# Kernel optimization log

Hardware: AMD Instinct MI355X
Metric: run time of the kernel (lower is better)

Reference implementation:

```python
import jax, jax.numpy as jnp
import numpy as np

N, CH, H, W = 4, 512, 64, 64
FEAT, NUM_K, POOL_PER = 256, 64, 128
POOL = NUM_K * POOL_PER  # 8192 total concept slots


def setup_inputs() -> dict:
    key = jax.random.key(0)
    k_x, k_t, k_o, k_p = jax.random.split(key, 4)
    x = jax.random.normal(k_x, (N, CH, H, W), dtype=jnp.float32)
    # 1x1 conv weights stored as [out, in] matrices (kernel_size=1, bias=False)
    w_theta = jax.random.normal(k_t, (FEAT, CH), dtype=jnp.float32) * 0.02
    w_o = jax.random.normal(k_o, (CH, FEAT), dtype=jnp.float32) * 0.02
    # concept pool buffer initialized with torch.rand -> uniform [0, 1)
    concept_pool = jax.random.uniform(k_p, (FEAT, POOL), dtype=jnp.float32)
    gamma = jnp.float32(0.5)  # learned scalar gate (init 0.0 in module; 0.5 to exercise the path)
    return {"x": x, "w_theta": w_theta, "w_o": w_o, "concept_pool": concept_pool, "gamma": gamma}


def reference(x, w_theta, w_o, concept_pool, gamma):
    # Concept attention: queries from theta 1x1 conv, keys/values are the
    # external concept pool memory [feature_dim, total_pool_size].
    n, c, h, w = x.shape
    hw = h * w
    # theta 1x1 conv: [n, ch, h, w] -> [n, feat, hw]
    theta = jnp.einsum('nchw,fc->nfhw', x, w_theta).reshape(n, FEAT, hw)
    # attention logits over pool slots: [n, hw, pool]
    logits = jnp.einsum('nfl,fp->nlp', theta, concept_pool)
    attn = jax.nn.softmax(logits, axis=-1)
    # aggregate pool values: [n, feat, hw]
    agg = jnp.einsum('nlp,fp->nfl', attn, concept_pool).reshape(n, FEAT, h, w)
    # output 1x1 conv back to ch, gated residual
    o = jnp.einsum('nfhw,cf->nchw', agg, w_o)
    return x + gamma * o
```

## Files before the change

kernel.cpp:

```cpp
#include <hip/hip_runtime.h>

#define NB 4
#define CHN 512
#define HWD 4096
#define LTOT (NB*HWD)
#define FEAT_ 256
#define POOL_ 8192

typedef __attribute__((ext_vector_type(8))) __bf16 bf16x8;
typedef __attribute__((ext_vector_type(8))) unsigned short u16x8;
typedef __attribute__((ext_vector_type(8))) _Float16 f16x8;
typedef __attribute__((ext_vector_type(4))) float f32x4;
typedef __attribute__((ext_vector_type(16))) float f32x16;

static __device__ __forceinline__ unsigned short f2bf(float f){
  union { float f; unsigned u; } c; c.f = f;
  unsigned u = c.u;
  u += 0x7fffu + ((u >> 16) & 1u);
  return (unsigned short)(u >> 16);
}

static __device__ __forceinline__ unsigned pk_f16(float lo, float hi){
  auto r = __builtin_amdgcn_cvt_pkrtz(lo, hi);
  return __builtin_bit_cast(unsigned, r);
}

static __device__ __forceinline__ f32x4 mfma16(bf16x8 a, bf16x8 b, f32x4 c){
  return __builtin_amdgcn_mfma_f32_16x16x32_bf16(a, b, c, 0, 0, 0);
}
static __device__ __forceinline__ f32x4 mfma16h(f16x8 a, f16x8 b, f32x4 c){
  return __builtin_amdgcn_mfma_f32_16x16x32_f16(a, b, c, 0, 0, 0);
}
static __device__ __forceinline__ f32x16 mfma32h(f16x8 a, f16x8 b, f32x16 c){
  return __builtin_amdgcn_mfma_f32_32x32x16_f16(a, b, c, 0, 0, 0);
}

static __device__ __forceinline__ bf16x8 ld_bf8(const void* p){
  u16x8 v = *(const u16x8*)p;
  return __builtin_bit_cast(bf16x8, v);
}
static __device__ __forceinline__ f16x8 ld_f8(const void* p){
  u16x8 v = *(const u16x8*)p;
  return __builtin_bit_cast(f16x8, v);
}

static __device__ __forceinline__ void gload16(const void* g, void* l){
  __builtin_amdgcn_global_load_lds((const __attribute__((address_space(1))) void*)g,
                                   (__attribute__((address_space(3))) void*)l, 16, 0, 0);
}

__global__ void k_cvt(const float* __restrict__ src, unsigned short* __restrict__ dst, int n4){
  int i = blockIdx.x * 256 + threadIdx.x;
  if (i < n4) {
    const float4 v = *(const float4*)(src + (size_t)i * 4);
    ushort4 o; o.x = f2bf(v.x); o.y = f2bf(v.y); o.z = f2bf(v.z); o.w = f2bf(v.w);
    *(ushort4*)(dst + (size_t)i * 4) = o;
  }
}

__global__ __launch_bounds__(256) void k_poolKF(const float* __restrict__ pool,
                                                unsigned short* __restrict__ poolKF){
  int t = blockIdx.x >> 2;
  int tid = threadIdx.x;
  int kk = ((blockIdx.x & 3) << 1) | (tid >> 7);
  int half = (tid >> 6) & 1;
  int lane = tid & 63;
  int p = t*32 + half*16 + (lane & 15);
  int f0 = kk*32 + ((lane >> 4) & 3)*8;
  u16x8 o;
  #pragma unroll
  for (int j = 0; j < 8; ++j) o[j] = f2bf(pool[(size_t)(f0+j)*POOL_ + p]);
  *(u16x8*)((char*)poolKF + (size_t)t*16384 + (kk*2+half)*1024 + lane*16) = o;
}

__global__ __launch_bounds__(256) void k_poolVF(const float* __restrict__ pool,
                                                _Float16* __restrict__ poolVF){
  int t = blockIdx.x >> 2;
  int tid = threadIdx.x;
  int g = ((blockIdx.x & 3) << 2) | (tid >> 6);
  int lane = tid & 63;
  int f = (g & 7)*32 + (lane & 31);
  int sb = ((g >> 3) << 4) + ((lane >> 5) << 3);
  f16x8 o;
  #pragma unroll
  for (int j = 0; j < 8; ++j) {
    int s = sb + j;
    int po = (s >> 1) + ((s & 1) << 4);
    o[j] = (_Float16)pool[(size_t)f*POOL_ + t*32 + po];
  }
  *(f16x8*)((char*)poolVF + (size_t)t*16384 + g*1024 + lane*16) = o;
}

__global__ __launch_bounds__(256) void k_xT(const float* __restrict__ x,
                                            unsigned short* __restrict__ xT){
  __shared__ float tile[32][33];
  int b = blockIdx.x;
  int lt = b & 127; int ct = (b >> 7) & 15; int n = b >> 11;
  int t = threadIdx.x;
  int fi = t >> 3, j = (t & 7) * 4;
  const float4 v = *(const float4*)(x + ((size_t)(n*CHN + ct*32 + fi)) * HWD + lt*32 + j);
  tile[fi][j+0] = v.x; tile[fi][j+1] = v.y; tile[fi][j+2] = v.z; tile[fi][j+3] = v.w;
  __syncthreads();
  int pi = t >> 3, fj = (t & 7) * 4;
  ushort4 o;
  o.x = f2bf(tile[fj+0][pi]); o.y = f2bf(tile[fj+1][pi]);
  o.z = f2bf(tile[fj+2][pi]); o.w = f2bf(tile[fj+3][pi]);
  *(ushort4*)((char*)xT + ((size_t)(n*HWD + lt*32 + pi)) * 1024 + (ct*32 + fj) * 2) = o;
}

__global__ __launch_bounds__(256) void k_theta(const unsigned short* __restrict__ xT,
                                               const unsigned short* __restrict__ wt,
                                               unsigned short* __restrict__ Q){
  int w = threadIdx.x >> 6, lane = threadIdx.x & 63;
  int lq = lane & 15, hq = lane >> 4;
  int lbase = blockIdx.x * 64 + w * 16;
  const char* xb = (const char*)xT;
  const char* wb = (const char*)wt;
  f32x4 acc[16];
  #pragma unroll
  for (int i = 0; i < 16; ++i) acc[i] = {};
  #pragma unroll 2
  for (int kk = 0; kk < 16; ++kk) {
    bf16x8 a = ld_bf8(xb + (size_t)(lbase + lq) * 1024 + kk*64 + hq*16);
    #pragma unroll
    for (int fi = 0; fi < 16; ++fi) {
      bf16x8 bfr = ld_bf8(wb + (size_t)(fi*16 + lq) * 1024 + kk*64 + hq*16);
      acc[fi] = mfma16(a, bfr, acc[fi]);
    }
  }
  #pragma unroll
  for (int fi = 0; fi < 16; ++fi) {
    #pragma unroll
    for (int r = 0; r < 4; ++r) {
      int l = lbase + hq*4 + r;
      Q[(size_t)l * 256 + fi*16 + lq] = f2bf(acc[fi][r]);
    }
  }
}

__global__ __launch_bounds__(256, 2) void k_attn(const unsigned short* __restrict__ Qg,
                                                 const unsigned short* __restrict__ poolKF,
                                                 const _Float16* __restrict__ poolVF,
                                                 _Float16* __restrict__ accP,
                                                 float* __restrict__ pm,
                                                 float* __restrict__ ps){
  __shared__ __attribute__((aligned(16))) unsigned short K_lds[2][32*256];
  __shared__ __attribute__((aligned(16))) _Float16 V_lds[2][8192];
  __shared__ __attribute__((aligned(16))) _Float16 P_lds[4][32][40];
  __shared__ float Sc[4][32];
  __shared__ float As[4][32];

  int w = threadIdx.x >> 6, lane = threadIdx.x & 63;
  int lq = lane & 15, hq = lane >> 4;
  int ln = lane & 31, h2 = lane >> 5;
  int qblock = blockIdx.x & 127, slice = blockIdx.x >> 7;
  int qa0 = qblock * 128 + w * 32;

  const char* qp = (const char*)Qg;
  bf16x8 qfa[8], qfb[8];
  #pragma unroll
  for (int kk = 0; kk < 8; ++kk) {
    qfa[kk] = ld_bf8(qp + (size_t)(qa0 + lq) * 512 + kk*64 + hq*16);
    qfb[kk] = ld_bf8(qp + (size_t)(qa0 + 16 + lq) * 512 + kk*64 + hq*16);
  }

  f32x16 acc32[8];
  #pragma unroll
  for (int i = 0; i < 8; ++i) acc32[i] = {};
  f32x4 accsA = {}, accsB = {};
  float ma0 = -__builtin_inff(), ma1 = -__builtin_inff(),
        ma2 = -__builtin_inff(), ma3 = -__builtin_inff();
  float mb0 = -__builtin_inff(), mb1 = -__builtin_inff(),
        mb2 = -__builtin_inff(), mb3 = -__builtin_inff();
  u16x8 ov;
  #pragma unroll
  for (int i = 0; i < 8; ++i) ov[i] = 0x3C00;
  const f16x8 ONESH = __builtin_bit_cast(f16x8, ov);

  const char* ktb = (const char*)poolKF;
  const char* vnb = (const char*)poolVF;
  int kds[4];
  #pragma unroll
  for (int i = 0; i < 4; ++i) kds[i] = (w*4 + i) * 1024;
  int lsrc = lane * 16;
  _Float16 (*Pw)[40] = P_lds[w];

  {
    size_t tb = (size_t)(slice * 64) * 16384;
    #pragma unroll
    for (int i = 0; i < 4; ++i) {
      gload16(ktb + tb + kds[i] + lsrc, (char*)K_lds[0] + kds[i]);
      gload16(vnb + tb + kds[i] + lsrc, (char*)V_lds[0] + kds[i]);
    }
  }
  __syncthreads();

  int cur = 0;
  for (int t = 0; t < 64; ++t) {
    if (t < 63) {
      size_t tb = (size_t)(slice*64 + t + 1) * 16384;
      #pragma unroll
      for (int i = 0; i < 4; ++i) {
        gload16(ktb + tb + kds[i] + lsrc, (char*)K_lds[cur^1] + kds[i]);
        gload16(vnb + tb + kds[i] + lsrc, (char*)V_lds[cur^1] + kds[i]);
      }
    }

    const char* Kb = (const char*)K_lds[cur] + lsrc;
    const char* Vb = (const char*)V_lds[cur] + lsrc;

    f32x4 s0a = {}, s1a = {}, s0b = {}, s1b = {};
    #pragma unroll
    for (int kk = 0; kk < 8; ++kk) {
      bf16x8 k0 = ld_bf8(Kb + kk*2048);
      bf16x8 k1 = ld_bf8(Kb + kk*2048 + 1024);
      s0a = mfma16(qfa[kk], k0, s0a);
      s1a = mfma16(qfa[kk], k1, s1a);
      s0b = mfma16(qfb[kk], k0, s0b);
      s1b = mfma16(qfb[kk], k1, s1b);
    }

    float pa0 = fmaxf(s0a[0], s1a[0]), pa1 = fmaxf(s0a[1], s1a[1]),
          pa2 = fmaxf(s0a[2], s1a[2]), pa3 = fmaxf(s0a[3], s1a[3]);
    float pb0 = fmaxf(s0b[0], s1b[0]), pb1 = fmaxf(s0b[1], s1b[1]),
          pb2 = fmaxf(s0b[2], s1b[2]), pb3 = fmaxf(s0b[3], s1b[3]);
    bool ex = (pa0 > ma0+4.f) | (pa1 > ma1+4.f) | (pa2 > ma2+4.f) | (pa3 > ma3+4.f) |
              (pb0 > mb0+4.f) | (pb1 > mb1+4.f) | (pb2 > mb2+4.f) | (pb3 > mb3+4.f);
    if (__any((int)ex)) {
      #pragma unroll
      for (int msk = 1; msk < 16; msk <<= 1) {
        pa0 = fmaxf(pa0, __shfl_xor(pa0, msk));
        pa1 = fmaxf(pa1, __shfl_xor(pa1, msk));
        pa2 = fmaxf(pa2, __shfl_xor(pa2, msk));
        pa3 = fmaxf(pa3, __shfl_xor(pa3, msk));
        pb0 = fmaxf(pb0, __shfl_xor(pb0, msk));
        pb1 = fmaxf(pb1, __shfl_xor(pb1, msk));
        pb2 = fmaxf(pb2, __shfl_xor(pb2, msk));
        pb3 = fmaxf(pb3, __shfl_xor(pb3, msk));
      }
      float na0 = fmaxf(ma0, pa0), na1 = fmaxf(ma1, pa1),
            na2 = fmaxf(ma2, pa2), na3 = fmaxf(ma3, pa3);
      float nb0 = fmaxf(mb0, pb0), nb1 = fmaxf(mb1, pb1),
            nb2 = fmaxf(mb2, pb2), nb3 = fmaxf(mb3, pb3);
      float sa0 = __expf(ma0 - na0), sa1 = __expf(ma1 - na1),
            sa2 = __expf(ma2 - na2), sa3 = __expf(ma3 - na3);
      float sb0 = __expf(mb0 - nb0), sb1 = __expf(mb1 - nb1),
            sb2 = __expf(mb2 - nb2), sb3 = __expf(mb3 - nb3);
      ma0 = na0; ma1 = na1; ma2 = na2; ma3 = na3;
      mb0 = nb0; mb1 = nb1; mb2 = nb2; mb3 = nb3;
      accsA[0] *= sa0; accsA[1] *= sa1; accsA[2] *= sa2; accsA[3] *= sa3;
      accsB[0] *= sb0; accsB[1] *= sb1; accsB[2] *= sb2; accsB[3] *= sb3;
      if (lq == 0) {
        Sc[w][4*hq+0] = sa0; Sc[w][4*hq+1] = sa1;
        Sc[w][4*hq+2] = sa2; Sc[w][4*hq+3] = sa3;
        Sc[w][16+4*hq+0] = sb0; Sc[w][16+4*hq+1] = sb1;
        Sc[w][16+4*hq+2] = sb2; Sc[w][16+4*hq+3] = sb3;
      }
      f32x4 s4[4];
      #pragma unroll
      for (int blk = 0; blk < 4; ++blk)
        s4[blk] = *(const f32x4*)&Sc[w][8*blk + 4*h2];
      #pragma unroll
      for (int fb = 0; fb < 8; ++fb)
        #pragma unroll
        for (int r = 0; r < 16; ++r)
          acc32[fb][r] *= s4[r>>2][r&3];
    }

    {
      int q0 = hq * 4;
      *(unsigned*)&Pw[q0+0][lq*2] = pk_f16(__expf(s0a[0]-ma0), __expf(s1a[0]-ma0));
      *(unsigned*)&Pw[q0+1][lq*2] = pk_f16(__expf(s0a[1]-ma1), __expf(s1a[1]-ma1));
      *(unsigned*)&Pw[q0+2][lq*2] = pk_f16(__expf(s0a[2]-ma2), __expf(s1a[2]-ma2));
      *(unsigned*)&Pw[q0+3][lq*2] = pk_f16(__expf(s0a[3]-ma3), __expf(s1a[3]-ma3));
      *(unsigned*)&Pw[16+q0+0][lq*2] = pk_f16(__expf(s0b[0]-mb0), __expf(s1b[0]-mb0));
      *(unsigned*)&Pw[16+q0+1][lq*2] = pk_f16(__expf(s0b[1]-mb1), __expf(s1b[1]-mb1));
      *(unsigned*)&Pw[16+q0+2][lq*2] = pk_f16(__expf(s0b[2]-mb2), __expf(s1b[2]-mb2));
      *(unsigned*)&Pw[16+q0+3][lq*2] = pk_f16(__expf(s0b[3]-mb3), __expf(s1b[3]-mb3));
    }

    f16x8 paA = ld_f8(&Pw[lq][hq*8]);
    f16x8 paB = ld_f8(&Pw[16+lq][hq*8]);
    accsA = mfma16h(paA, ONESH, accsA);
    accsB = mfma16h(paB, ONESH, accsB);

    #pragma unroll
    for (int ph = 0; ph < 2; ++ph) {
      f16x8 pfrag = ld_f8(&Pw[ln][ph*16 + h2*8]);
      #pragma unroll
      for (int fb = 0; fb < 8; ++fb) {
        f16x8 vfrag = ld_f8(Vb + (ph*8 + fb)*1024);
        acc32[fb] = mfma32h(pfrag, vfrag, acc32[fb]);
      }
    }

    __syncthreads();
    cur ^= 1;
  }

  if (lq == 0) {
    As[w][4*hq+0] = accsA[0]; As[w][4*hq+1] = accsA[1];
    As[w][4*hq+2] = accsA[2]; As[w][4*hq+3] = accsA[3];
    As[w][16+4*hq+0] = accsB[0]; As[w][16+4*hq+1] = accsB[1];
    As[w][16+4*hq+2] = accsB[2]; As[w][16+4*hq+3] = accsB[3];
  }
  float inv[16];
  #pragma unroll
  for (int blk = 0; blk < 4; ++blk) {
    f32x4 a4 = *(const f32x4*)&As[w][8*blk + 4*h2];
    inv[blk*4+0] = 1.0f / a4[0]; inv[blk*4+1] = 1.0f / a4[1];
    inv[blk*4+2] = 1.0f / a4[2]; inv[blk*4+3] = 1.0f / a4[3];
  }
  size_t sbase = (size_t)slice * 16384 + qa0;
  #pragma unroll
  for (int fb = 0; fb < 8; ++fb) {
    #pragma unroll
    for (int r = 0; r < 16; ++r) {
      int q = (r & 3) + 8*(r >> 2) + 4*h2;
      accP[(sbase + q) * 256 + fb*32 + ln] = (_Float16)(acc32[fb][r] * inv[r]);
    }
  }
  if (lq == 0) {
    pm[sbase + 4*hq + 0] = ma0; ps[sbase + 4*hq + 0] = accsA[0];
    pm[sbase + 4*hq + 1] = ma1; ps[sbase + 4*hq + 1] = accsA[1];
    pm[sbase + 4*hq + 2] = ma2; ps[sbase + 4*hq + 2] = accsA[2];
    pm[sbase + 4*hq + 3] = ma3; ps[sbase + 4*hq + 3] = accsA[3];
    pm[sbase + 16 + 4*hq + 0] = mb0; ps[sbase + 16 + 4*hq + 0] = accsB[0];
    pm[sbase + 16 + 4*hq + 1] = mb1; ps[sbase + 16 + 4*hq + 1] = accsB[1];
    pm[sbase + 16 + 4*hq + 2] = mb2; ps[sbase + 16 + 4*hq + 2] = accsB[2];
    pm[sbase + 16 + 4*hq + 3] = mb3; ps[sbase + 16 + 4*hq + 3] = accsB[3];
  }
}

__global__ __launch_bounds__(256) void k_comb(const _Float16* __restrict__ accP,
                                              const float* __restrict__ pm,
                                              const float* __restrict__ ps,
                                              unsigned short* __restrict__ agg){
  int q = blockIdx.x * 16 + (threadIdx.x >> 4);
  int f0 = (threadIdx.x & 15) * 16;
  float m0 = pm[q], m1 = pm[16384 + q], m2 = pm[2*16384 + q], m3 = pm[3*16384 + q];
  float M = fmaxf(fmaxf(m0, m1), fmaxf(m2, m3));
  float w0 = __expf(m0 - M) * ps[q];
  float w1 = __expf(m1 - M) * ps[16384 + q];
  float w2 = __expf(m2 - M) * ps[2*16384 + q];
  float w3 = __expf(m3 - M) * ps[3*16384 + q];
  float inv = 1.0f / (w0 + w1 + w2 + w3);
  w0 *= inv; w1 *= inv; w2 *= inv; w3 *= inv;
  const _Float16* a0 = accP + (size_t)q * 256 + f0;
  #pragma unroll
  for (int j = 0; j < 16; j += 8) {
    f16x8 v0 = *(const f16x8*)(a0 + j);
    f16x8 v1 = *(const f16x8*)(a0 + j + (size_t)16384*256);
    f16x8 v2 = *(const f16x8*)(a0 + j + (size_t)2*16384*256);
    f16x8 v3 = *(const f16x8*)(a0 + j + (size_t)3*16384*256);
    u16x8 o;
    #pragma unroll
    for (int k = 0; k < 8; ++k) {
      float s = w0*(float)v0[k] + w1*(float)v1[k] + w2*(float)v2[k] + w3*(float)v3[k];
      o[k] = f2bf(s);
    }
    *(u16x8*)(agg + (size_t)q * 256 + f0 + j) = o;
  }
}

__global__ __launch_bounds__(256) void k_out(const float* __restrict__ x,
                                             const unsigned short* __restrict__ wo,
                                             const unsigned short* __restrict__ agg,
                                             const float* __restrict__ gammap,
                                             float* __restrict__ out){
  int w = threadIdx.x >> 6, lane = threadIdx.x & 63;
  int lq = lane & 15, hq = lane >> 4;
  int b = blockIdx.x;
  int lg = b & 63, cg = (b >> 6) & 7, n = b >> 9;
  const char* wb = (const char*)wo;
  const char* ab = (const char*)agg;
  f32x4 acc[4];
  #pragma unroll
  for (int i = 0; i < 4; ++i) acc[i] = {};
  int crow = cg*64 + w*16 + lq;
  #pragma unroll
  for (int kk = 0; kk < 8; ++kk) {
    bf16x8 a = ld_bf8(wb + (size_t)crow * 512 + kk*64 + hq*16);
    #pragma unroll
    for (int li = 0; li < 4; ++li) {
      bf16x8 bb = ld_bf8(ab + (size_t)(n*HWD + lg*64 + li*16 + lq) * 512 + kk*64 + hq*16);
      acc[li] = mfma16(a, bb, acc[li]);
    }
  }
  float g = gammap[0];
  #pragma unroll
  for (int li = 0; li < 4; ++li) {
    #pragma unroll
    for (int r = 0; r < 4; ++r) {
      int c = cg*64 + w*16 + hq*4 + r;
      int l = lg*64 + li*16 + lq;
      size_t idx = ((size_t)(n*CHN + c)) * HWD + l;
      out[idx] = x[idx] + g * acc[li][r];
    }
  }
}

extern "C" void kernel_launch(void* const* d_in, const int* in_sizes, int n_in,
                              void* d_out, int out_size, void* d_ws, size_t ws_size,
                              hipStream_t stream) {
  const float* x     = (const float*)d_in[0];
  const float* wt    = (const float*)d_in[1];
  const float* wo    = (const float*)d_in[2];
  const float* pool  = (const float*)d_in[3];
  const float* gamma = (const float*)d_in[4];
  char* ws = (char*)d_ws;
  unsigned short* wt_b  = (unsigned short*)(ws + 0);
  unsigned short* wo_b  = (unsigned short*)(ws + 262144);
  _Float16*       poolVF= (_Float16*)(ws + 524288);
  unsigned short* poolKF= (unsigned short*)(ws + 4718592);
  unsigned short* Qb    = (unsigned short*)(ws + 8912896);
  unsigned short* aggb  = (unsigned short*)(ws + 17301504);
  unsigned short* xT    = (unsigned short*)(ws + 25690112);
  _Float16*       accP  = (_Float16*)(ws + 25690112);
  float*          pm    = (float*)(ws + 59244544);
  float*          ps    = (float*)(ws + 59506688);
  float* out = (float*)d_out;

  k_cvt<<<dim3(128), dim3(256), 0, stream>>>(wt, wt_b, 32768);
  k_cvt<<<dim3(128), dim3(256), 0, stream>>>(wo, wo_b, 32768);
  k_poolVF<<<dim3(1024), dim3(256), 0, stream>>>(pool, poolVF);
  k_poolKF<<<dim3(1024), dim3(256), 0, stream>>>(pool, poolKF);
  k_xT<<<dim3(8192), dim3(256), 0, stream>>>(x, xT);
  k_theta<<<dim3(256), dim3(256), 0, stream>>>(xT, wt_b, Qb);
  k_attn<<<dim3(512), dim3(256), 0, stream>>>(Qb, poolKF, poolVF, accP, pm, ps);
  k_comb<<<dim3(1024), dim3(256), 0, stream>>>(accP, pm, ps, aggb);
  k_out<<<dim3(2048), dim3(256), 0, stream>>>(x, wo_b, aggb, gamma, out);
}
```

Before: 258.7 us.

## Compute S^T with 32x32 MFMA so P stays in registers, use exp2

Restructures the attention inner loop to compute transposed scores with 32x32x16 bf16 MFMA, K as the A operand and Q as B. Each lane then holds one query's scores, so softmax row max and sum need only one cross-half shuffle. Probabilities are packed straight into f16 registers as the A operand for the PV MFMA, which removes the P round trip through LDS and the ones-vector MFMA row-sum. Pool K/V pre-layouts are changed to match, and log2(e) is folded into Q so exp2 replaces expf. This cuts LDS traffic and shuffles, at the cost of a different rescale threshold and extra VALU summation.

```diff
diff --git a/kernel.cpp b/kernel.cpp
--- a/kernel.cpp
+++ b/kernel.cpp
@@ -10,8 +10,13 @@
 typedef __attribute__((ext_vector_type(8))) __bf16 bf16x8;
 typedef __attribute__((ext_vector_type(8))) unsigned short u16x8;
 typedef __attribute__((ext_vector_type(8))) _Float16 f16x8;
+typedef __attribute__((ext_vector_type(4))) unsigned u32x4;
 typedef __attribute__((ext_vector_type(4))) float f32x4;
 typedef __attribute__((ext_vector_type(16))) float f32x16;
+
+static __device__ __forceinline__ float fexp2(float x){
+  return __builtin_amdgcn_exp2f(x);
+}
 
 static __device__ __forceinline__ unsigned short f2bf(float f){
   union { float f; unsigned u; } c; c.f = f;
@@ -28,8 +33,8 @@
 static __device__ __forceinline__ f32x4 mfma16(bf16x8 a, bf16x8 b, f32x4 c){
   return __builtin_amdgcn_mfma_f32_16x16x32_bf16(a, b, c, 0, 0, 0);
 }
-static __device__ __forceinline__ f32x4 mfma16h(f16x8 a, f16x8 b, f32x4 c){
-  return __builtin_amdgcn_mfma_f32_16x16x32_f16(a, b, c, 0, 0, 0);
+static __device__ __forceinline__ f32x16 mfma32b(bf16x8 a, bf16x8 b, f32x16 c){
+  return __builtin_amdgcn_mfma_f32_32x32x16_bf16(a, b, c, 0, 0, 0);
 }
 static __device__ __forceinline__ f32x16 mfma32h(f16x8 a, f16x8 b, f32x16 c){
   return __builtin_amdgcn_mfma_f32_32x32x16_f16(a, b, c, 0, 0, 0);
@@ -62,15 +67,14 @@
                                                 unsigned short* __restrict__ poolKF){
   int t = blockIdx.x >> 2;
   int tid = threadIdx.x;
-  int kk = ((blockIdx.x & 3) << 1) | (tid >> 7);
-  int half = (tid >> 6) & 1;
+  int kc = ((blockIdx.x & 3) << 2) | (tid >> 6);
   int lane = tid & 63;
-  int p = t*32 + half*16 + (lane & 15);
-  int f0 = kk*32 + ((lane >> 4) & 3)*8;
+  int p = t*32 + (lane & 31);
+  int f0 = kc*16 + (lane >> 5)*8;
   u16x8 o;
   #pragma unroll
   for (int j = 0; j < 8; ++j) o[j] = f2bf(pool[(size_t)(f0+j)*POOL_ + p]);
-  *(u16x8*)((char*)poolKF + (size_t)t*16384 + (kk*2+half)*1024 + lane*16) = o;
+  *(u16x8*)((char*)poolKF + (size_t)t*16384 + kc*1024 + lane*16) = o;
 }
 
 __global__ __launch_bounds__(256) void k_poolVF(const float* __restrict__ pool,
@@ -80,12 +84,11 @@
   int g = ((blockIdx.x & 3) << 2) | (tid >> 6);
   int lane = tid & 63;
   int f = (g & 7)*32 + (lane & 31);
-  int sb = ((g >> 3) << 4) + ((lane >> 5) << 3);
+  int ph = g >> 3, h2 = lane >> 5;
   f16x8 o;
   #pragma unroll
   for (int j = 0; j < 8; ++j) {
-    int s = sb + j;
-    int po = (s >> 1) + ((s & 1) << 4);
+    int po = (j & 3) + 8*(j >> 2) + 4*h2 + 16*ph;
     o[j] = (_Float16)pool[(size_t)f*POOL_ + t*32 + po];
   }
   *(f16x8*)((char*)poolVF + (size_t)t*16384 + g*1024 + lane*16) = o;
@@ -133,7 +136,7 @@
     #pragma unroll
     for (int r = 0; r < 4; ++r) {
       int l = lbase + hq*4 + r;
-      Q[(size_t)l * 256 + fi*16 + lq] = f2bf(acc[fi][r]);
+      Q[(size_t)l * 256 + fi*16 + lq] = f2bf(acc[fi][r] * 1.44269504f);
     }
   }
 }
@@ -146,36 +149,25 @@
                                                  float* __restrict__ ps){
   __shared__ __attribute__((aligned(16))) unsigned short K_lds[2][32*256];
   __shared__ __attribute__((aligned(16))) _Float16 V_lds[2][8192];
-  __shared__ __attribute__((aligned(16))) _Float16 P_lds[4][32][40];
   __shared__ float Sc[4][32];
   __shared__ float As[4][32];
 
   int w = threadIdx.x >> 6, lane = threadIdx.x & 63;
-  int lq = lane & 15, hq = lane >> 4;
   int ln = lane & 31, h2 = lane >> 5;
   int qblock = blockIdx.x & 127, slice = blockIdx.x >> 7;
   int qa0 = qblock * 128 + w * 32;
 
   const char* qp = (const char*)Qg;
-  bf16x8 qfa[8], qfb[8];
-  #pragma unroll
-  for (int kk = 0; kk < 8; ++kk) {
-    qfa[kk] = ld_bf8(qp + (size_t)(qa0 + lq) * 512 + kk*64 + hq*16);
-    qfb[kk] = ld_bf8(qp + (size_t)(qa0 + 16 + lq) * 512 + kk*64 + hq*16);
-  }
+  bf16x8 qf[16];
+  #pragma unroll
+  for (int kc = 0; kc < 16; ++kc)
+    qf[kc] = ld_bf8(qp + (size_t)(qa0 + ln) * 512 + kc*32 + h2*16);
 
   f32x16 acc32[8];
   #pragma unroll
   for (int i = 0; i < 8; ++i) acc32[i] = {};
-  f32x4 accsA = {}, accsB = {};
-  float ma0 = -__builtin_inff(), ma1 = -__builtin_inff(),
-        ma2 = -__builtin_inff(), ma3 = -__builtin_inff();
-  float mb0 = -__builtin_inff(), mb1 = -__builtin_inff(),
-        mb2 = -__builtin_inff(), mb3 = -__builtin_inff();
-  u16x8 ov;
-  #pragma unroll
-  for (int i = 0; i < 8; ++i) ov[i] = 0x3C00;
-  const f16x8 ONESH = __builtin_bit_cast(f16x8, ov);
+  float accs = 0.0f;
+  float m = -__builtin_inff();
 
   const char* ktb = (const char*)poolKF;
   const char* vnb = (const char*)poolVF;
@@ -183,7 +175,6 @@
   #pragma unroll
   for (int i = 0; i < 4; ++i) kds[i] = (w*4 + i) * 1024;
   int lsrc = lane * 16;
-  _Float16 (*Pw)[40] = P_lds[w];
 
   {
     size_t tb = (size_t)(slice * 64) * 16384;
@@ -209,53 +200,29 @@
     const char* Kb = (const char*)K_lds[cur] + lsrc;
     const char* Vb = (const char*)V_lds[cur] + lsrc;
 
-    f32x4 s0a = {}, s1a = {}, s0b = {}, s1b = {};
-    #pragma unroll
-    for (int kk = 0; kk < 8; ++kk) {
-      bf16x8 k0 = ld_bf8(Kb + kk*2048);
-      bf16x8 k1 = ld_bf8(Kb + kk*2048 + 1024);
-      s0a = mfma16(qfa[kk], k0, s0a);
-      s1a = mfma16(qfa[kk], k1, s1a);
-      s0b = mfma16(qfb[kk], k0, s0b);
-      s1b = mfma16(qfb[kk], k1, s1b);
-    }
-
-    float pa0 = fmaxf(s0a[0], s1a[0]), pa1 = fmaxf(s0a[1], s1a[1]),
-          pa2 = fmaxf(s0a[2], s1a[2]), pa3 = fmaxf(s0a[3], s1a[3]);
-    float pb0 = fmaxf(s0b[0], s1b[0]), pb1 = fmaxf(s0b[1], s1b[1]),
-          pb2 = fmaxf(s0b[2], s1b[2]), pb3 = fmaxf(s0b[3], s1b[3]);
-    bool ex = (pa0 > ma0+4.f) | (pa1 > ma1+4.f) | (pa2 > ma2+4.f) | (pa3 > ma3+4.f) |
-              (pb0 > mb0+4.f) | (pb1 > mb1+4.f) | (pb2 > mb2+4.f) | (pb3 > mb3+4.f);
-    if (__any((int)ex)) {
-      #pragma unroll
-      for (int msk = 1; msk < 16; msk <<= 1) {
-        pa0 = fmaxf(pa0, __shfl_xor(pa0, msk));
-        pa1 = fmaxf(pa1, __shfl_xor(pa1, msk));
-        pa2 = fmaxf(pa2, __shfl_xor(pa2, msk));
-        pa3 = fmaxf(pa3, __shfl_xor(pa3, msk));
-        pb0 = fmaxf(pb0, __shfl_xor(pb0, msk));
-        pb1 = fmaxf(pb1, __shfl_xor(pb1, msk));
-        pb2 = fmaxf(pb2, __shfl_xor(pb2, msk));
-        pb3 = fmaxf(pb3, __shfl_xor(pb3, msk));
-      }
-      float na0 = fmaxf(ma0, pa0), na1 = fmaxf(ma1, pa1),
-            na2 = fmaxf(ma2, pa2), na3 = fmaxf(ma3, pa3);
-      float nb0 = fmaxf(mb0, pb0), nb1 = fmaxf(mb1, pb1),
-            nb2 = fmaxf(mb2, pb2), nb3 = fmaxf(mb3, pb3);
-      float sa0 = __expf(ma0 - na0), sa1 = __expf(ma1 - na1),
-            sa2 = __expf(ma2 - na2), sa3 = __expf(ma3 - na3);
-      float sb0 = __expf(mb0 - nb0), sb1 = __expf(mb1 - nb1),
-            sb2 = __expf(mb2 - nb2), sb3 = __expf(mb3 - nb3);
-      ma0 = na0; ma1 = na1; ma2 = na2; ma3 = na3;
-      mb0 = nb0; mb1 = nb1; mb2 = nb2; mb3 = nb3;
-      accsA[0] *= sa0; accsA[1] *= sa1; accsA[2] *= sa2; accsA[3] *= sa3;
-      accsB[0] *= sb0; accsB[1] *= sb1; accsB[2] *= sb2; accsB[3] *= sb3;
-      if (lq == 0) {
-        Sc[w][4*hq+0] = sa0; Sc[w][4*hq+1] = sa1;
-        Sc[w][4*hq+2] = sa2; Sc[w][4*hq+3] = sa3;
-        Sc[w][16+4*hq+0] = sb0; Sc[w][16+4*hq+1] = sb1;
-        Sc[w][16+4*hq+2] = sb2; Sc[w][16+4*hq+3] = sb3;
-      }
+    f32x16 Sa = {}, Sb = {};
+    #pragma unroll
+    for (int kc = 0; kc < 8; ++kc) {
+      bf16x8 k0 = ld_bf8(Kb + (2*kc)*1024);
+      bf16x8 k1 = ld_bf8(Kb + (2*kc+1)*1024);
+      Sa = mfma32b(k0, qf[2*kc], Sa);
+      Sb = mfma32b(k1, qf[2*kc+1], Sb);
+    }
+    float S[16];
+    #pragma unroll
+    for (int r = 0; r < 16; ++r) S[r] = Sa[r] + Sb[r];
+
+    float px = S[0];
+    #pragma unroll
+    for (int r = 1; r < 16; ++r) px = fmaxf(px, S[r]);
+    px = fmaxf(px, __shfl_xor(px, 32));
+
+    if (__any((int)(px > m + 5.5f))) {
+      float mn = fmaxf(m, px);
+      float sc = fexp2(m - mn);
+      m = mn;
+      accs *= sc;
+      if (lane < 32) Sc[w][lane] = sc;
       f32x4 s4[4];
       #pragma unroll
       for (int blk = 0; blk < 4; ++blk)
@@ -267,43 +234,38 @@
           acc32[fb][r] *= s4[r>>2][r&3];
     }
 
-    {
-      int q0 = hq * 4;
-      *(unsigned*)&Pw[q0+0][lq*2] = pk_f16(__expf(s0a[0]-ma0), __expf(s1a[0]-ma0));
-      *(unsigned*)&Pw[q0+1][lq*2] = pk_f16(__expf(s0a[1]-ma1), __expf(s1a[1]-ma1));
-      *(unsigned*)&Pw[q0+2][lq*2] = pk_f16(__expf(s0a[2]-ma2), __expf(s1a[2]-ma2));
-      *(unsigned*)&Pw[q0+3][lq*2] = pk_f16(__expf(s0a[3]-ma3), __expf(s1a[3]-ma3));
-      *(unsigned*)&Pw[16+q0+0][lq*2] = pk_f16(__expf(s0b[0]-mb0), __expf(s1b[0]-mb0));
-      *(unsigned*)&Pw[16+q0+1][lq*2] = pk_f16(__expf(s0b[1]-mb1), __expf(s1b[1]-mb1));
-      *(unsigned*)&Pw[16+q0+2][lq*2] = pk_f16(__expf(s0b[2]-mb2), __expf(s1b[2]-mb2));
-      *(unsigned*)&Pw[16+q0+3][lq*2] = pk_f16(__expf(s0b[3]-mb3), __expf(s1b[3]-mb3));
-    }
-
-    f16x8 paA = ld_f8(&Pw[lq][hq*8]);
-    f16x8 paB = ld_f8(&Pw[16+lq][hq*8]);
-    accsA = mfma16h(paA, ONESH, accsA);
-    accsB = mfma16h(paB, ONESH, accsB);
-
-    #pragma unroll
-    for (int ph = 0; ph < 2; ++ph) {
-      f16x8 pfrag = ld_f8(&Pw[ln][ph*16 + h2*8]);
-      #pragma unroll
-      for (int fb = 0; fb < 8; ++fb) {
-        f16x8 vfrag = ld_f8(Vb + (ph*8 + fb)*1024);
-        acc32[fb] = mfma32h(pfrag, vfrag, acc32[fb]);
-      }
+    float Pr[16];
+    #pragma unroll
+    for (int r = 0; r < 16; ++r) Pr[r] = fexp2(S[r] - m);
+    float sum = (((Pr[0]+Pr[1])+(Pr[2]+Pr[3])) + ((Pr[4]+Pr[5])+(Pr[6]+Pr[7])))
+              + (((Pr[8]+Pr[9])+(Pr[10]+Pr[11])) + ((Pr[12]+Pr[13])+(Pr[14]+Pr[15])));
+    sum += __shfl_xor(sum, 32);
+    accs += sum;
+    u32x4 w0, w1;
+    #pragma unroll
+    for (int j = 0; j < 4; ++j) {
+      w0[j] = pk_f16(Pr[2*j],   Pr[2*j+1]);
+      w1[j] = pk_f16(Pr[8+2*j], Pr[8+2*j+1]);
+    }
+    f16x8 pa0 = __builtin_bit_cast(f16x8, w0);
+    f16x8 pa1 = __builtin_bit_cast(f16x8, w1);
+
+    #pragma unroll
+    for (int fb = 0; fb < 8; ++fb) {
+      f16x8 v0 = ld_f8(Vb + fb*1024);
+      acc32[fb] = mfma32h(pa0, v0, acc32[fb]);
+    }
+    #pragma unroll
+    for (int fb = 0; fb < 8; ++fb) {
+      f16x8 v1 = ld_f8(Vb + (8 + fb)*1024);
+      acc32[fb] = mfma32h(pa1, v1, acc32[fb]);
     }
 
     __syncthreads();
     cur ^= 1;
   }
 
-  if (lq == 0) {
-    As[w][4*hq+0] = accsA[0]; As[w][4*hq+1] = accsA[1];
-    As[w][4*hq+2] = accsA[2]; As[w][4*hq+3] = accsA[3];
-    As[w][16+4*hq+0] = accsB[0]; As[w][16+4*hq+1] = accsB[1];
-    As[w][16+4*hq+2] = accsB[2]; As[w][16+4*hq+3] = accsB[3];
-  }
+  if (lane < 32) As[w][lane] = accs;
   float inv[16];
   #pragma unroll
   for (int blk = 0; blk < 4; ++blk) {
@@ -320,15 +282,9 @@
       accP[(sbase + q) * 256 + fb*32 + ln] = (_Float16)(acc32[fb][r] * inv[r]);
     }
   }
-  if (lq == 0) {
-    pm[sbase + 4*hq + 0] = ma0; ps[sbase + 4*hq + 0] = accsA[0];
-    pm[sbase + 4*hq + 1] = ma1; ps[sbase + 4*hq + 1] = accsA[1];
-    pm[sbase + 4*hq + 2] = ma2; ps[sbase + 4*hq + 2] = accsA[2];
-    pm[sbase + 4*hq + 3] = ma3; ps[sbase + 4*hq + 3] = accsA[3];
-    pm[sbase + 16 + 4*hq + 0] = mb0; ps[sbase + 16 + 4*hq + 0] = accsB[0];
-    pm[sbase + 16 + 4*hq + 1] = mb1; ps[sbase + 16 + 4*hq + 1] = accsB[1];
-    pm[sbase + 16 + 4*hq + 2] = mb2; ps[sbase + 16 + 4*hq + 2] = accsB[2];
-    pm[sbase + 16 + 4*hq + 3] = mb3; ps[sbase + 16 + 4*hq + 3] = accsB[3];
+  if (lane < 32) {
+    pm[sbase + lane] = m;
+    ps[sbase + lane] = accs;
   }
 }
 
@@ -340,10 +296,10 @@
   int f0 = (threadIdx.x & 15) * 16;
   float m0 = pm[q], m1 = pm[16384 + q], m2 = pm[2*16384 + q], m3 = pm[3*16384 + q];
   float M = fmaxf(fmaxf(m0, m1), fmaxf(m2, m3));
-  float w0 = __expf(m0 - M) * ps[q];
-  float w1 = __expf(m1 - M) * ps[16384 + q];
-  float w2 = __expf(m2 - M) * ps[2*16384 + q];
-  float w3 = __expf(m3 - M) * ps[3*16384 + q];
+  float w0 = fexp2(m0 - M) * ps[q];
+  float w1 = fexp2(m1 - M) * ps[16384 + q];
+  float w2 = fexp2(m2 - M) * ps[2*16384 + q];
+  float w3 = fexp2(m3 - M) * ps[3*16384 + q];
   float inv = 1.0f / (w0 + w1 + w2 + w3);
   w0 *= inv; w1 *= inv; w2 *= inv; w3 *= inv;
   const _Float16* a0 = accP + (size_t)q * 256 + f0;
```

After: 246.5 us. 4.7% less time.
